# Kernel tuning notes

Hardware: AMD Instinct MI355X
Metric: run time of the kernel (lower is better)

Reference implementation:

```python
import jax, jax.numpy as jnp
import numpy as np

N_NODES = 100000
N_EDGES = 1600000
D_FEAT = 64
EPS = 1e-07


def setup_inputs() -> dict:
    key = jax.random.key(0)
    k1, k2, k3 = jax.random.split(key, 3)
    x = jax.random.normal(k1, (N_NODES, D_FEAT), dtype=jnp.float32)
    beta = jnp.ones((1,), dtype=jnp.float32)
    edge_row = jnp.sort(jax.random.randint(k2, (N_EDGES,), 0, N_NODES, dtype=jnp.int64))
    edge_col = jax.random.randint(k3, (N_EDGES,), 0, N_NODES, dtype=jnp.int64)
    return {"x": x, "beta": beta, "edge_row": edge_row, "edge_col": edge_col}


def reference(x, beta, edge_row, edge_col):
    # Gather endpoint features: [E, d]
    A = x[edge_row]
    B = x[edge_col]
    # Cosine similarity per edge, scaled by beta: [E]
    inner = jnp.sum(A * B, axis=1)
    norms = jnp.linalg.norm(A, axis=1) * jnp.linalg.norm(B, axis=1)
    sim = beta[0] * (inner / (norms + EPS))
    # Sparse row-wise softmax (tf.sparse.softmax): stable segment softmax over edges grouped by row
    row_max = jax.ops.segment_max(sim, edge_row, num_segments=N_NODES)
    e = jnp.exp(sim - row_max[edge_row])
    row_sum = jax.ops.segment_sum(e, edge_row, num_segments=N_NODES)
    p = e / row_sum[edge_row]  # [E]
    # SPMM: out[i] = sum_{(i,j) in E} p_ij * x[j]
    out = jax.ops.segment_sum(p[:, None] * B, edge_row, num_segments=N_NODES)
    return out
```

## Files before the change

### kernel.cpp

```cpp
#include <hip/hip_runtime.h>
#include <math.h>

#define D_FEAT 64
typedef _Float16 v8h __attribute__((ext_vector_type(8)));
typedef _Float16 v4h __attribute__((ext_vector_type(4)));
typedef float v4f __attribute__((ext_vector_type(4)));

static __device__ __forceinline__ v8h u2h8(uint4 u){ v8h v; __builtin_memcpy(&v,&u,16); return v; }
static __device__ __forceinline__ v4h u2h4(uint2 u){ v4h v; __builtin_memcpy(&v,&u,8); return v; }
static __device__ __forceinline__ float f16lo(unsigned int m){
    unsigned short us = (unsigned short)(m & 0xffffu);
    _Float16 h; __builtin_memcpy(&h, &us, 2); return (float)h;
}

__global__ __launch_bounds__(256)
void agnn_prep1(const float* __restrict__ x, float* __restrict__ nf,
                uint2* __restrict__ xh, int n_nodes) {
    int t = blockIdx.x*blockDim.x + threadIdx.x;
    int node = t >> 4; if (node >= n_nodes) return;
    int l4 = t & 15;
    float4 v = ((const float4*)x)[node*16 + l4];
    float ss = v.x*v.x + v.y*v.y + v.z*v.z + v.w*v.w;
    #pragma unroll
    for (int off = 1; off < 16; off <<= 1) ss += __shfl_xor(ss, off, 64);
    float r = ss > 0.f ? rsqrtf(ss) : 0.f;
    if (l4 == 0) nf[node] = ss * r;
    auto h0 = __builtin_amdgcn_cvt_pkrtz(v.x*r, v.y*r);
    auto h1 = __builtin_amdgcn_cvt_pkrtz(v.z*r, v.w*r);
    uint2 u; __builtin_memcpy(&u.x, &h0, 4); __builtin_memcpy(&u.y, &h1, 4);
    xh[node*16 + l4] = u;
}

__global__ __launch_bounds__(256)
void agnn_prep2(const int* __restrict__ edge_row, const int* __restrict__ edge_col,
                const float* __restrict__ nf, int* __restrict__ row_ptr,
                unsigned int* __restrict__ md, int n_nodes, int n_edges) {
    int e = blockIdx.x*blockDim.x + threadIdx.x;
    if (e < 64) md[n_edges + e] = 0xFFFF0000u;
    if (e >= n_edges) return;
    int r1 = edge_row[e];
    int r0 = (e == 0) ? -1 : edge_row[e-1];
    for (int r = r0+1; r <= r1; ++r) row_ptr[r] = e;
    if (e == n_edges-1)
        for (int r = r1+1; r <= n_nodes; ++r) row_ptr[r] = n_edges;
    _Float16 h = (_Float16)nf[edge_col[e]];
    unsigned short us; __builtin_memcpy(&us, &h, 2);
    md[e] = ((unsigned int)(r1 & 15) << 16) | us;
}

#define XCP_PITCH 144
#define WAVE_LDS_B (32 * XCP_PITCH)
__global__ __launch_bounds__(256)
void agnn_fused(const float* __restrict__ beta_p,
                const int* __restrict__ edge_col,
                const unsigned int* __restrict__ md,
                const int* __restrict__ row_ptr,
                const uint4* __restrict__ xh4,
                float* __restrict__ out, int n_nodes) {
    __shared__ __align__(16) char lds_raw[4 * WAVE_LDS_B];
    int wid = threadIdx.x >> 6, lane = threadIdx.x & 63;
    int q = lane >> 4, lo4 = lane & 15;
    int sub = wid & 1;
    char* XCP = lds_raw + wid * WAVE_LDS_B;

    int tile = blockIdx.x*2 + (wid >> 1);
    int t0 = tile * 16;
    bool tile_ok = t0 < n_nodes;

    int qn = t0 + lo4;
    if (qn >= n_nodes) qn = n_nodes - 1;
    if (qn < 0) qn = 0;
    v8h b0 = u2h8(xh4[(size_t)qn*8 + q]);
    v8h b1 = u2h8(xh4[(size_t)qn*8 + 4 + q]);
    float beta  = beta_p[0];
    float shift = fabsf(beta);

    int es = 0, L = 0;
    if (tile_ok) {
        int te = t0 + 16; if (te > n_nodes) te = n_nodes;
        es = row_ptr[t0];
        L  = row_ptr[te] - es;
    }

    v4f o0={0,0,0,0}, o1={0,0,0,0}, o2={0,0,0,0}, o3={0,0,0,0};
    float s = 0.f;
    unsigned int selp = (lo4 & 1) ? 0x07060302u : 0x05040100u;

    for (int base = sub*32; base < L; base += 64) {
        int i0 = base + lo4;
        int e0 = es + (i0 < L ? i0 : 0);
        int i1 = base + 16 + lo4;
        int e1 = es + (i1 < L ? i1 : 0);
        int c0 = edge_col[e0];
        int c1 = edge_col[e1];
        uint4 A00 = xh4[(size_t)c0*8 + q];
        uint4 A01 = xh4[(size_t)c0*8 + 4 + q];
        uint4 A10 = xh4[(size_t)c1*8 + q];
        uint4 A11 = xh4[(size_t)c1*8 + 4 + q];
        int mb = es + base + 4*q;
        unsigned int m00 = md[mb+0],  m01 = md[mb+1],  m02 = md[mb+2],  m03 = md[mb+3];
        unsigned int m10 = md[mb+16], m11 = md[mb+17], m12 = md[mb+18], m13 = md[mb+19];

        v4f z0 = {0,0,0,0};
        z0 = __builtin_amdgcn_mfma_f32_16x16x32_f16(u2h8(A00), b0, z0, 0,0,0);
        z0 = __builtin_amdgcn_mfma_f32_16x16x32_f16(u2h8(A01), b1, z0, 0,0,0);
        v4f z1 = {0,0,0,0};
        z1 = __builtin_amdgcn_mfma_f32_16x16x32_f16(u2h8(A10), b0, z1, 0,0,0);
        z1 = __builtin_amdgcn_mfma_f32_16x16x32_f16(u2h8(A11), b1, z1, 0,0,0);

        {
            unsigned int colA = lo4*4, colB = (16+lo4)*4;
            char* pA = XCP + (4*q)*XCP_PITCH;
            char* pB = XCP + (16+4*q)*XCP_PITCH;
            *(unsigned int*)(pA + 0*XCP_PITCH + colA) = A00.x;
            *(unsigned int*)(pA + 1*XCP_PITCH + colA) = A00.y;
            *(unsigned int*)(pA + 2*XCP_PITCH + colA) = A00.z;
            *(unsigned int*)(pA + 3*XCP_PITCH + colA) = A00.w;
            *(unsigned int*)(pB + 0*XCP_PITCH + colA) = A01.x;
            *(unsigned int*)(pB + 1*XCP_PITCH + colA) = A01.y;
            *(unsigned int*)(pB + 2*XCP_PITCH + colA) = A01.z;
            *(unsigned int*)(pB + 3*XCP_PITCH + colA) = A01.w;
            *(unsigned int*)(pA + 0*XCP_PITCH + colB) = A10.x;
            *(unsigned int*)(pA + 1*XCP_PITCH + colB) = A10.y;
            *(unsigned int*)(pA + 2*XCP_PITCH + colB) = A10.z;
            *(unsigned int*)(pA + 3*XCP_PITCH + colB) = A10.w;
            *(unsigned int*)(pB + 0*XCP_PITCH + colB) = A11.x;
            *(unsigned int*)(pB + 1*XCP_PITCH + colB) = A11.y;
            *(unsigned int*)(pB + 2*XCP_PITCH + colB) = A11.z;
            *(unsigned int*)(pB + 3*XCP_PITCH + colB) = A11.w;
        }

        int lim0 = L - base - 4*q;
        int lim1 = lim0 - 16;
        float w00 = (0 < lim0 && (m00>>16)==(unsigned)lo4) ? __expf(fmaf(beta, z0[0], -shift)) : 0.f;
        float w01 = (1 < lim0 && (m01>>16)==(unsigned)lo4) ? __expf(fmaf(beta, z0[1], -shift)) : 0.f;
        float w02 = (2 < lim0 && (m02>>16)==(unsigned)lo4) ? __expf(fmaf(beta, z0[2], -shift)) : 0.f;
        float w03 = (3 < lim0 && (m03>>16)==(unsigned)lo4) ? __expf(fmaf(beta, z0[3], -shift)) : 0.f;
        float w10 = (0 < lim1 && (m10>>16)==(unsigned)lo4) ? __expf(fmaf(beta, z1[0], -shift)) : 0.f;
        float w11 = (1 < lim1 && (m11>>16)==(unsigned)lo4) ? __expf(fmaf(beta, z1[1], -shift)) : 0.f;
        float w12 = (2 < lim1 && (m12>>16)==(unsigned)lo4) ? __expf(fmaf(beta, z1[2], -shift)) : 0.f;
        float w13 = (3 < lim1 && (m13>>16)==(unsigned)lo4) ? __expf(fmaf(beta, z1[3], -shift)) : 0.f;
        s += (w00+w01) + (w02+w03) + (w10+w11) + (w12+w13);

        v4h pa0, pa1;
        {
            auto a = __builtin_amdgcn_cvt_pkrtz(w00*f16lo(m00), w01*f16lo(m01));
            auto b = __builtin_amdgcn_cvt_pkrtz(w02*f16lo(m02), w03*f16lo(m03));
            pa0[0]=a[0]; pa0[1]=a[1]; pa0[2]=b[0]; pa0[3]=b[1];
            auto c = __builtin_amdgcn_cvt_pkrtz(w10*f16lo(m10), w11*f16lo(m11));
            auto d = __builtin_amdgcn_cvt_pkrtz(w12*f16lo(m12), w13*f16lo(m13));
            pa1[0]=c[0]; pa1[1]=c[1]; pa1[2]=d[0]; pa1[3]=d[1];
        }

        const char* rbase_p = XCP + (lo4>>1)*XCP_PITCH + 16*q;
        {
            const char* rp = rbase_p;
            uint4 d0 = *(const uint4*)rp;
            uint4 d1 = *(const uint4*)(rp + 64);
            uint2 bb0 = { __builtin_amdgcn_perm(d0.y, d0.x, selp), __builtin_amdgcn_perm(d0.w, d0.z, selp) };
            uint2 bb1 = { __builtin_amdgcn_perm(d1.y, d1.x, selp), __builtin_amdgcn_perm(d1.w, d1.z, selp) };
            o0 = __builtin_amdgcn_mfma_f32_16x16x16f16(pa0, u2h4(bb0), o0, 0,0,0);
            o0 = __builtin_amdgcn_mfma_f32_16x16x16f16(pa1, u2h4(bb1), o0, 0,0,0);
        }
        {
            const char* rp = rbase_p + 8*XCP_PITCH;
            uint4 d0 = *(const uint4*)rp;
            uint4 d1 = *(const uint4*)(rp + 64);
            uint2 bb0 = { __builtin_amdgcn_perm(d0.y, d0.x, selp), __builtin_amdgcn_perm(d0.w, d0.z, selp) };
            uint2 bb1 = { __builtin_amdgcn_perm(d1.y, d1.x, selp), __builtin_amdgcn_perm(d1.w, d1.z, selp) };
            o1 = __builtin_amdgcn_mfma_f32_16x16x16f16(pa0, u2h4(bb0), o1, 0,0,0);
            o1 = __builtin_amdgcn_mfma_f32_16x16x16f16(pa1, u2h4(bb1), o1, 0,0,0);
        }
        {
            const char* rp = rbase_p + 16*XCP_PITCH;
            uint4 d0 = *(const uint4*)rp;
            uint4 d1 = *(const uint4*)(rp + 64);
            uint2 bb0 = { __builtin_amdgcn_perm(d0.y, d0.x, selp), __builtin_amdgcn_perm(d0.w, d0.z, selp) };
            uint2 bb1 = { __builtin_amdgcn_perm(d1.y, d1.x, selp), __builtin_amdgcn_perm(d1.w, d1.z, selp) };
            o2 = __builtin_amdgcn_mfma_f32_16x16x16f16(pa0, u2h4(bb0), o2, 0,0,0);
            o2 = __builtin_amdgcn_mfma_f32_16x16x16f16(pa1, u2h4(bb1), o2, 0,0,0);
        }
        {
            const char* rp = rbase_p + 24*XCP_PITCH;
            uint4 d0 = *(const uint4*)rp;
            uint4 d1 = *(const uint4*)(rp + 64);
            uint2 bb0 = { __builtin_amdgcn_perm(d0.y, d0.x, selp), __builtin_amdgcn_perm(d0.w, d0.z, selp) };
            uint2 bb1 = { __builtin_amdgcn_perm(d1.y, d1.x, selp), __builtin_amdgcn_perm(d1.w, d1.z, selp) };
            o3 = __builtin_amdgcn_mfma_f32_16x16x16f16(pa0, u2h4(bb0), o3, 0,0,0);
            o3 = __builtin_amdgcn_mfma_f32_16x16x16f16(pa1, u2h4(bb1), o3, 0,0,0);
        }
    }

    if (sub == 1) {
        float* cb = (float*)(lds_raw + wid * WAVE_LDS_B);
        #pragma unroll
        for (int r = 0; r < 4; ++r) {
            cb[(0*4+r)*64 + lane] = o0[r];
            cb[(1*4+r)*64 + lane] = o1[r];
            cb[(2*4+r)*64 + lane] = o2[r];
            cb[(3*4+r)*64 + lane] = o3[r];
        }
        cb[16*64 + lane] = s;
    }
    __syncthreads();
    if (sub == 0 && tile_ok) {
        const float* cb = (const float*)(lds_raw + (wid + 1) * WAVE_LDS_B);
        #pragma unroll
        for (int r = 0; r < 4; ++r) {
            o0[r] += cb[(0*4+r)*64 + lane];
            o1[r] += cb[(1*4+r)*64 + lane];
            o2[r] += cb[(2*4+r)*64 + lane];
            o3[r] += cb[(3*4+r)*64 + lane];
        }
        s += cb[16*64 + lane];

        s += __shfl_xor(s, 16, 64);
        s += __shfl_xor(s, 32, 64);

        #pragma unroll
        for (int r = 0; r < 4; ++r) {
            float sr = __shfl(s, 4*q + r, 64);
            float inv = sr > 0.f ? 1.f/sr : 0.f;
            int node = t0 + 4*q + r;
            if (node < n_nodes) {
                float* p = out + (size_t)node*64 + lo4;
                p[0]  = o0[r]*inv;
                p[16] = o1[r]*inv;
                p[32] = o2[r]*inv;
                p[48] = o3[r]*inv;
            }
        }
    }
}

extern "C" void kernel_launch(void* const* d_in, const int* in_sizes, int n_in,
                              void* d_out, int out_size, void* d_ws, size_t ws_size,
                              hipStream_t stream) {
    const float* x        = (const float*)d_in[0];
    const float* beta     = (const float*)d_in[1];
    const int*   edge_row = (const int*)d_in[2];
    const int*   edge_col = (const int*)d_in[3];
    float* out = (float*)d_out;

    int n_nodes = in_sizes[0] / D_FEAT;
    int n_edges = in_sizes[2];

    char* ws = (char*)d_ws;
    float* nf = (float*)ws;
    size_t off0 = ((size_t)n_nodes*sizeof(float) + 255) & ~(size_t)255;
    int* row_ptr = (int*)(ws + off0);
    size_t off1 = off0 + (((size_t)(n_nodes+1)*sizeof(int) + 255) & ~(size_t)255);
    unsigned int* md = (unsigned int*)(ws + off1);
    size_t off2 = off1 + (((size_t)(n_edges+64)*sizeof(unsigned int) + 255) & ~(size_t)255);
    uint2* xh = (uint2*)(ws + off2);

    {
        long long threads = (long long)n_nodes * 16;
        int blocks = (int)((threads + 255) / 256);
        agnn_prep1<<<blocks, 256, 0, stream>>>(x, nf, xh, n_nodes);
    }
    {
        int blocks = (n_edges + 255) / 256;
        agnn_prep2<<<blocks, 256, 0, stream>>>(edge_row, edge_col, nf, row_ptr,
                                               md, n_nodes, n_edges);
    }
    {
        int tiles  = (n_nodes + 15) / 16;
        int blocks = (tiles + 1) / 2;
        agnn_fused<<<blocks, 256, 0, stream>>>(beta, edge_col, md, row_ptr,
                                               (const uint4*)xh, out, n_nodes);
    }
}
```

Before: 137.8 us.

## Halve per-wave LDS staging by splitting edge halves and raise occupancy bound

The fused kernel now stages only one 16-edge half of the gathered neighbour features in LDS at a time, instead of both halves. This shrinks the per-wave row pitch from 144 to 80 bytes and reorders the SPMM MFMAs to consume each half before the next is written. The cross-wave reduction buffer now spans two wave regions, so an extra barrier is added before it is reused. The launch bound asks for 8 blocks per CU to raise occupancy, but that caps registers and risks spills, and the split adds LDS write-to-read serialisation within each wave.

```diff
diff --git a/kernel.cpp b/kernel.cpp
--- a/kernel.cpp
+++ b/kernel.cpp
@@ -48,9 +48,9 @@
     md[e] = ((unsigned int)(r1 & 15) << 16) | us;
 }
 
-#define XCP_PITCH 144
+#define XCP_PITCH 80
 #define WAVE_LDS_B (32 * XCP_PITCH)
-__global__ __launch_bounds__(256)
+__global__ __launch_bounds__(256, 8)
 void agnn_fused(const float* __restrict__ beta_p,
                 const int* __restrict__ edge_col,
                 const unsigned int* __restrict__ md,
@@ -108,28 +108,6 @@
         z1 = __builtin_amdgcn_mfma_f32_16x16x32_f16(u2h8(A10), b0, z1, 0,0,0);
         z1 = __builtin_amdgcn_mfma_f32_16x16x32_f16(u2h8(A11), b1, z1, 0,0,0);
 
-        {
-            unsigned int colA = lo4*4, colB = (16+lo4)*4;
-            char* pA = XCP + (4*q)*XCP_PITCH;
-            char* pB = XCP + (16+4*q)*XCP_PITCH;
-            *(unsigned int*)(pA + 0*XCP_PITCH + colA) = A00.x;
-            *(unsigned int*)(pA + 1*XCP_PITCH + colA) = A00.y;
-            *(unsigned int*)(pA + 2*XCP_PITCH + colA) = A00.z;
-            *(unsigned int*)(pA + 3*XCP_PITCH + colA) = A00.w;
-            *(unsigned int*)(pB + 0*XCP_PITCH + colA) = A01.x;
-            *(unsigned int*)(pB + 1*XCP_PITCH + colA) = A01.y;
-            *(unsigned int*)(pB + 2*XCP_PITCH + colA) = A01.z;
-            *(unsigned int*)(pB + 3*XCP_PITCH + colA) = A01.w;
-            *(unsigned int*)(pA + 0*XCP_PITCH + colB) = A10.x;
-            *(unsigned int*)(pA + 1*XCP_PITCH + colB) = A10.y;
-            *(unsigned int*)(pA + 2*XCP_PITCH + colB) = A10.z;
-            *(unsigned int*)(pA + 3*XCP_PITCH + colB) = A10.w;
-            *(unsigned int*)(pB + 0*XCP_PITCH + colB) = A11.x;
-            *(unsigned int*)(pB + 1*XCP_PITCH + colB) = A11.y;
-            *(unsigned int*)(pB + 2*XCP_PITCH + colB) = A11.z;
-            *(unsigned int*)(pB + 3*XCP_PITCH + colB) = A11.w;
-        }
-
         int lim0 = L - base - 4*q;
         int lim1 = lim0 - 16;
         float w00 = (0 < lim0 && (m00>>16)==(unsigned)lo4) ? __expf(fmaf(beta, z0[0], -shift)) : 0.f;
@@ -152,47 +130,67 @@
             pa1[0]=c[0]; pa1[1]=c[1]; pa1[2]=d[0]; pa1[3]=d[1];
         }
 
-        const char* rbase_p = XCP + (lo4>>1)*XCP_PITCH + 16*q;
-        {
-            const char* rp = rbase_p;
-            uint4 d0 = *(const uint4*)rp;
-            uint4 d1 = *(const uint4*)(rp + 64);
+        {
+            unsigned int col = lo4*4;
+            char* pA = XCP + (4*q)*XCP_PITCH;
+            char* pB = XCP + (16+4*q)*XCP_PITCH;
+            *(unsigned int*)(pA + 0*XCP_PITCH + col) = A00.x;
+            *(unsigned int*)(pA + 1*XCP_PITCH + col) = A00.y;
+            *(unsigned int*)(pA + 2*XCP_PITCH + col) = A00.z;
+            *(unsigned int*)(pA + 3*XCP_PITCH + col) = A00.w;
+            *(unsigned int*)(pB + 0*XCP_PITCH + col) = A01.x;
+            *(unsigned int*)(pB + 1*XCP_PITCH + col) = A01.y;
+            *(unsigned int*)(pB + 2*XCP_PITCH + col) = A01.z;
+            *(unsigned int*)(pB + 3*XCP_PITCH + col) = A01.w;
+        }
+        {
+            const char* rbp = XCP + (lo4>>1)*XCP_PITCH + 16*q;
+            uint4 d0 = *(const uint4*)(rbp + 0*XCP_PITCH*8);
+            uint4 d1 = *(const uint4*)(rbp + 8*XCP_PITCH);
+            uint4 d2 = *(const uint4*)(rbp + 16*XCP_PITCH);
+            uint4 d3 = *(const uint4*)(rbp + 24*XCP_PITCH);
             uint2 bb0 = { __builtin_amdgcn_perm(d0.y, d0.x, selp), __builtin_amdgcn_perm(d0.w, d0.z, selp) };
             uint2 bb1 = { __builtin_amdgcn_perm(d1.y, d1.x, selp), __builtin_amdgcn_perm(d1.w, d1.z, selp) };
+            uint2 bb2 = { __builtin_amdgcn_perm(d2.y, d2.x, selp), __builtin_amdgcn_perm(d2.w, d2.z, selp) };
+            uint2 bb3 = { __builtin_amdgcn_perm(d3.y, d3.x, selp), __builtin_amdgcn_perm(d3.w, d3.z, selp) };
             o0 = __builtin_amdgcn_mfma_f32_16x16x16f16(pa0, u2h4(bb0), o0, 0,0,0);
-            o0 = __builtin_amdgcn_mfma_f32_16x16x16f16(pa1, u2h4(bb1), o0, 0,0,0);
-        }
-        {
-            const char* rp = rbase_p + 8*XCP_PITCH;
-            uint4 d0 = *(const uint4*)rp;
-            uint4 d1 = *(const uint4*)(rp + 64);
+            o1 = __builtin_amdgcn_mfma_f32_16x16x16f16(pa0, u2h4(bb1), o1, 0,0,0);
+            o2 = __builtin_amdgcn_mfma_f32_16x16x16f16(pa0, u2h4(bb2), o2, 0,0,0);
+            o3 = __builtin_amdgcn_mfma_f32_16x16x16f16(pa0, u2h4(bb3), o3, 0,0,0);
+        }
+        {
+            unsigned int col = lo4*4;
+            char* pA = XCP + (4*q)*XCP_PITCH;
+            char* pB = XCP + (16+4*q)*XCP_PITCH;
+            *(unsigned int*)(pA + 0*XCP_PITCH + col) = A10.x;
+            *(unsigned int*)(pA + 1*XCP_PITCH + col) = A10.y;
+            *(unsigned int*)(pA + 2*XCP_PITCH + col) = A10.z;
+            *(unsigned int*)(pA + 3*XCP_PITCH + col) = A10.w;
+            *(unsigned int*)(pB + 0*XCP_PITCH + col) = A11.x;
+            *(unsigned int*)(pB + 1*XCP_PITCH + col) = A11.y;
+            *(unsigned int*)(pB + 2*XCP_PITCH + col) = A11.z;
+            *(unsigned int*)(pB + 3*XCP_PITCH + col) = A11.w;
+        }
+        {
+            const char* rbp = XCP + (lo4>>1)*XCP_PITCH + 16*q;
+            uint4 d0 = *(const uint4*)(rbp + 0*XCP_PITCH*8);
+            uint4 d1 = *(const uint4*)(rbp + 8*XCP_PITCH);
+            uint4 d2 = *(const uint4*)(rbp + 16*XCP_PITCH);
+            uint4 d3 = *(const uint4*)(rbp + 24*XCP_PITCH);
             uint2 bb0 = { __builtin_amdgcn_perm(d0.y, d0.x, selp), __builtin_amdgcn_perm(d0.w, d0.z, selp) };
             uint2 bb1 = { __builtin_amdgcn_perm(d1.y, d1.x, selp), __builtin_amdgcn_perm(d1.w, d1.z, selp) };
-            o1 = __builtin_amdgcn_mfma_f32_16x16x16f16(pa0, u2h4(bb0), o1, 0,0,0);
+            uint2 bb2 = { __builtin_amdgcn_perm(d2.y, d2.x, selp), __builtin_amdgcn_perm(d2.w, d2.z, selp) };
+            uint2 bb3 = { __builtin_amdgcn_perm(d3.y, d3.x, selp), __builtin_amdgcn_perm(d3.w, d3.z, selp) };
+            o0 = __builtin_amdgcn_mfma_f32_16x16x16f16(pa1, u2h4(bb0), o0, 0,0,0);
             o1 = __builtin_amdgcn_mfma_f32_16x16x16f16(pa1, u2h4(bb1), o1, 0,0,0);
-        }
-        {
-            const char* rp = rbase_p + 16*XCP_PITCH;
-            uint4 d0 = *(const uint4*)rp;
-            uint4 d1 = *(const uint4*)(rp + 64);
-            uint2 bb0 = { __builtin_amdgcn_perm(d0.y, d0.x, selp), __builtin_amdgcn_perm(d0.w, d0.z, selp) };
-            uint2 bb1 = { __builtin_amdgcn_perm(d1.y, d1.x, selp), __builtin_amdgcn_perm(d1.w, d1.z, selp) };
-            o2 = __builtin_amdgcn_mfma_f32_16x16x16f16(pa0, u2h4(bb0), o2, 0,0,0);
-            o2 = __builtin_amdgcn_mfma_f32_16x16x16f16(pa1, u2h4(bb1), o2, 0,0,0);
-        }
-        {
-            const char* rp = rbase_p + 24*XCP_PITCH;
-            uint4 d0 = *(const uint4*)rp;
-            uint4 d1 = *(const uint4*)(rp + 64);
-            uint2 bb0 = { __builtin_amdgcn_perm(d0.y, d0.x, selp), __builtin_amdgcn_perm(d0.w, d0.z, selp) };
-            uint2 bb1 = { __builtin_amdgcn_perm(d1.y, d1.x, selp), __builtin_amdgcn_perm(d1.w, d1.z, selp) };
-            o3 = __builtin_amdgcn_mfma_f32_16x16x16f16(pa0, u2h4(bb0), o3, 0,0,0);
-            o3 = __builtin_amdgcn_mfma_f32_16x16x16f16(pa1, u2h4(bb1), o3, 0,0,0);
-        }
-    }
-
+            o2 = __builtin_amdgcn_mfma_f32_16x16x16f16(pa1, u2h4(bb2), o2, 0,0,0);
+            o3 = __builtin_amdgcn_mfma_f32_16x16x16f16(pa1, u2h4(bb3), o3, 0,0,0);
+        }
+    }
+
+    __syncthreads();
     if (sub == 1) {
-        float* cb = (float*)(lds_raw + wid * WAVE_LDS_B);
+        float* cb = (float*)(lds_raw + (wid - 1) * WAVE_LDS_B);
         #pragma unroll
         for (int r = 0; r < 4; ++r) {
             cb[(0*4+r)*64 + lane] = o0[r];
@@ -204,7 +202,7 @@
     }
     __syncthreads();
     if (sub == 0 && tile_ok) {
-        const float* cb = (const float*)(lds_raw + (wid + 1) * WAVE_LDS_B);
+        const float* cb = (const float*)(lds_raw + wid * WAVE_LDS_B);
         #pragma unroll
         for (int r = 0; r < 4; ++r) {
             o0[r] += cb[(0*4+r)*64 + lane];
```

New measurement: 163.0 us. +18.3%, slower.
